# Performance work log

Measured on AMD Instinct MI355X. Metric: run time of the kernel, lower is better.

The kernel has to match this reference:

```python
import jax, jax.numpy as jnp
import numpy as np
import itertools

B, N, C, D = 2, 150000, 64, 128  # samples, points/sample, channels, voxel grid extent
EPS = 1e-4  # BatchNormBlock eps
# 3x3x3 submanifold kernel offsets (27 taps)
OFFS = jnp.array(list(itertools.product((-1, 0, 1), repeat=3)), dtype=jnp.int32)  # [27,3]


def setup_inputs() -> dict:
    key = jax.random.key(0)
    k1, k2 = jax.random.split(key)
    rng = np.random.default_rng(0)
    # unique voxel coordinates per sample on a D^3 grid
    pos = np.stack([
        np.stack(np.unravel_index(rng.choice(D ** 3, size=N, replace=False), (D, D, D)), axis=-1)
        for _ in range(B)
    ]).astype(np.int32)  # [B,N,3]
    feats = jax.random.normal(k1, (B, N, C), jnp.float32)
    # 4 submanifold convs (2 residual blocks x 2 convs), fan-in scaled
    Ws = jax.random.normal(k2, (4, 27, C, C), jnp.float32) / np.sqrt(27 * C)
    gammas = jnp.ones((4, C), jnp.float32)
    betas = jnp.zeros((4, C), jnp.float32)
    return {"feats": feats, "Ws": Ws, "gammas": gammas, "betas": betas, "pos": jnp.asarray(pos)}


def _build_lut(pos_b):  # pos_b: [N,3] int32 -> dense hash grid [D^3] of point index or -1
    code = (pos_b[:, 0] * D + pos_b[:, 1]) * D + pos_b[:, 2]
    return jnp.full((D ** 3,), -1, jnp.int32).at[code].set(jnp.arange(N, dtype=jnp.int32))


def _subconv(x, lut_b, pos_b, W):
    # submanifold sparse conv: per kernel tap, gather neighbor features and GEMM
    # x:[N,C], lut_b:[D^3], pos_b:[N,3], W:[27,Cin,Cout]
    def step(acc, kw):
        d, Wk = kw
        npos = pos_b + d  # [N,3]
        valid = jnp.all((npos >= 0) & (npos < D), axis=-1)
        code = (npos[:, 0] * D + npos[:, 1]) * D + npos[:, 2]
        nidx = lut_b[jnp.where(valid, code, 0)]
        valid = valid & (nidx >= 0)
        g = jnp.where(valid[:, None], x[jnp.clip(nidx, 0, N - 1)], 0.0)  # [N,Cin]
        return acc + g @ Wk, None

    acc0 = jnp.zeros((x.shape[0], W.shape[-1]), x.dtype)
    acc, _ = jax.lax.scan(step, acc0, (OFFS, W))
    return acc


def _bn_relu(x, g, b):
    # BatchNormBlock (train mode, biased var over all concatenated points) + ReLU
    mu = x.mean(axis=(0, 1))
    var = jnp.mean(jnp.square(x - mu), axis=(0, 1))
    return jax.nn.relu((x - mu) * jax.lax.rsqrt(var + EPS) * g + b)


def reference(feats, Ws, gammas, betas, pos):
    lut = jax.vmap(_build_lut)(pos)  # [B, D^3]
    conv = jax.vmap(_subconv, in_axes=(0, 0, 0, None))
    x = feats
    for blk in range(2):  # conv_block_reps ResidualBlocks (NIN is Identity since nIn==nOut)
        out1 = x
        h = _bn_relu(x, gammas[2 * blk], betas[2 * blk])
        h = conv(h, lut, pos, Ws[2 * blk])
        h = _bn_relu(h, gammas[2 * blk + 1], betas[2 * blk + 1])
        out2 = conv(h, lut, pos, Ws[2 * blk + 1])
        x = out1 + out2
    return x
```

## Files before the change

### kernel.cpp

```cpp
#include <hip/hip_runtime.h>
#include <stdint.h>

#define DGRID 128
#define D3 (DGRID * DGRID * DGRID)
#define NBATCH 2
#define NPTS 150000
#define NROWS (NBATCH * NPTS)
#define NPAD 300032
#define ZROW NROWS
#define NCBLK (NPAD / 256)
#define EPSBN 1e-4f
#define SBLK 1024

typedef __attribute__((ext_vector_type(8))) short s16x8;
typedef __attribute__((ext_vector_type(4))) float f32x4;

static __device__ __forceinline__ uint32_t f2bf_rne(float f) {
  uint32_t b = __float_as_uint(f);
  return (b + 0x7FFFu + ((b >> 16) & 1u)) >> 16;
}

static __device__ __forceinline__ f32x4 mfma16(uint4 a, uint4 b, f32x4 c) {
  return __builtin_amdgcn_mfma_f32_16x16x32_bf16(
      __builtin_bit_cast(s16x8, a), __builtin_bit_cast(s16x8, b), c, 0, 0, 0);
}

__global__ void k_scatter(const int* __restrict__ pos, int* __restrict__ lut) {
  int g = blockIdx.x * blockDim.x + threadIdx.x;
  if (g >= NROWS) return;
  int b = g / NPTS;
  int i = g - b * NPTS;
  int x = pos[3 * g], y = pos[3 * g + 1], z = pos[3 * g + 2];
  lut[(size_t)b * D3 + (x * DGRID + y) * DGRID + z] = i;
}

__global__ void k_nbr(const int* __restrict__ pos, const int* __restrict__ lut,
                      int* __restrict__ nbr) {
  int g = blockIdx.x * blockDim.x + threadIdx.x;
  if (g >= NPAD) return;
  if (g >= NROWS) {
#pragma unroll
    for (int t = 0; t < 27; ++t) nbr[(size_t)t * NPAD + g] = ZROW;
    return;
  }
  int b = g / NPTS;
  int x = pos[3 * g], y = pos[3 * g + 1], z = pos[3 * g + 2];
  const int* L = lut + (size_t)b * D3;
#pragma unroll
  for (int t = 0; t < 27; ++t) {
    int nx = x + t / 9 - 1;
    int ny = y + (t / 3) % 3 - 1;
    int nz = z + t % 3 - 1;
    int v = ZROW;
    if ((unsigned)nx < DGRID && (unsigned)ny < DGRID && (unsigned)nz < DGRID) {
      int n = L[(nx * DGRID + ny) * DGRID + nz];
      if (n >= 0) v = b * NPTS + n;
    }
    nbr[(size_t)t * NPAD + g] = v;
  }
}

__global__ void k_wpack(const float* __restrict__ Ws, uint4* __restrict__ Wfrag) {
  int e = blockIdx.x * 256 + threadIdx.x;
  if (e >= 4 * 27 * 512) return;
  int lane = e & 63, nb = (e >> 6) & 3, s = (e >> 8) & 1, tt = e >> 9;
  int kb = s * 32 + (lane >> 4) * 8;
  int cout = nb * 16 + (lane & 15);
  const float* src = Ws + (size_t)tt * 4096;
  uint32_t p[4];
#pragma unroll
  for (int j = 0; j < 4; ++j) {
    uint32_t lo = f2bf_rne(src[(kb + 2 * j) * 64 + cout]);
    uint32_t hi = f2bf_rne(src[(kb + 2 * j + 1) * 64 + cout]);
    p[j] = (hi << 16) | lo;
  }
  uint4 o;
  o.x = p[0]; o.y = p[1]; o.z = p[2]; o.w = p[3];
  Wfrag[e] = o;
}

__global__ void k_stats1(const float* __restrict__ X, float* __restrict__ part) {
  __shared__ float s[512];
  int c = threadIdx.x & 63, q = threadIdx.x >> 6;
  float sm = 0.f, sq = 0.f;
  for (int r = blockIdx.x * 4 + q; r < NROWS; r += SBLK * 4) {
    float v = X[(size_t)r * 64 + c];
    sm += v;
    sq += v * v;
  }
  s[threadIdx.x] = sm;
  s[256 + threadIdx.x] = sq;
  __syncthreads();
  if (q == 0) {
    sm = s[c] + s[64 + c] + s[128 + c] + s[192 + c];
    sq = s[256 + c] + s[320 + c] + s[384 + c] + s[448 + c];
    part[blockIdx.x * 128 + c] = sm;
    part[blockIdx.x * 128 + 64 + c] = sq;
  }
}

__global__ void k_stats2(const float* __restrict__ part, int nblk,
                         const float* __restrict__ gamma, const float* __restrict__ beta,
                         float* __restrict__ chanp, int cid) {
  __shared__ float s[512];
  int c = threadIdx.x & 63, q = threadIdx.x >> 6;
  float sm = 0.f, sq = 0.f;
  for (int rb = q; rb < nblk; rb += 4) {
    sm += part[rb * 128 + c];
    sq += part[rb * 128 + 64 + c];
  }
  s[threadIdx.x] = sm;
  s[256 + threadIdx.x] = sq;
  __syncthreads();
  if (q == 0) {
    sm = s[c] + s[64 + c] + s[128 + c] + s[192 + c];
    sq = s[256 + c] + s[320 + c] + s[384 + c] + s[448 + c];
    float mean = sm / (float)NROWS;
    float var = sq / (float)NROWS - mean * mean;
    float a = gamma[cid * 64 + c] * rsqrtf(var + EPSBN);
    chanp[cid * 128 + c] = a;
    chanp[cid * 128 + 64 + c] = beta[cid * 64 + c] - mean * a;
  }
}

__global__ void k_hpass(const float* __restrict__ X, const float* __restrict__ chanp,
                        int cid, uint4* __restrict__ h) {
  int g = blockIdx.x * blockDim.x + threadIdx.x;
  if (g >= (NROWS + 1) * 8) return;
  if (g >= NROWS * 8) {
    h[g] = (uint4){0u, 0u, 0u, 0u};
    return;
  }
  int c0 = (g & 7) * 8;
  const float* cp = chanp + cid * 128;
  const float4 a0 = *(const float4*)(cp + c0);
  const float4 a1 = *(const float4*)(cp + c0 + 4);
  const float4 b0 = *(const float4*)(cp + 64 + c0);
  const float4 b1 = *(const float4*)(cp + 64 + c0 + 4);
  const float4 x0 = *(const float4*)(X + (size_t)g * 8);
  const float4 x1 = *(const float4*)(X + (size_t)g * 8 + 4);
  float v0 = fmaxf(fmaf(x0.x, a0.x, b0.x), 0.f);
  float v1 = fmaxf(fmaf(x0.y, a0.y, b0.y), 0.f);
  float v2 = fmaxf(fmaf(x0.z, a0.z, b0.z), 0.f);
  float v3 = fmaxf(fmaf(x0.w, a0.w, b0.w), 0.f);
  float v4 = fmaxf(fmaf(x1.x, a1.x, b1.x), 0.f);
  float v5 = fmaxf(fmaf(x1.y, a1.y, b1.y), 0.f);
  float v6 = fmaxf(fmaf(x1.z, a1.z, b1.z), 0.f);
  float v7 = fmaxf(fmaf(x1.w, a1.w, b1.w), 0.f);
  uint4 o;
  o.x = (f2bf_rne(v1) << 16) | f2bf_rne(v0);
  o.y = (f2bf_rne(v3) << 16) | f2bf_rne(v2);
  o.z = (f2bf_rne(v5) << 16) | f2bf_rne(v4);
  o.w = (f2bf_rne(v7) << 16) | f2bf_rne(v6);
  h[g] = o;
}

#define MFMA_HALF(AREG, WOFF)                                            \
  {                                                                      \
    uint4 wf[4];                                                         \
    _Pragma("unroll") for (int nb = 0; nb < 4; nb++) wf[nb] =            \
        Wt[(WOFF) + nb * 64];                                            \
    _Pragma("unroll") for (int rt = 0; rt < 4; rt++)                     \
        _Pragma("unroll") for (int nb = 0; nb < 4; nb++) acc[rt][nb] =   \
            mfma16(AREG, wf[nb], acc[rt][nb]);                           \
  }

__global__ __launch_bounds__(256) void k_conv(
    const uint4* __restrict__ h, const uint4* __restrict__ Wf,
    const int* __restrict__ nbr, const float* __restrict__ res,
    float* __restrict__ out, float* __restrict__ part, int do_stats) {
  __shared__ float xp[4][16 * 68];
  __shared__ float sred[2][4][4][16];
  int tid = threadIdx.x, wv = tid >> 6, lane = tid & 63;
  int tbase = (blockIdx.x * 4 + wv) * 64;
  int lrow = lane & 15, lkg = lane >> 4;

  f32x4 acc[4][4];
#pragma unroll
  for (int i = 0; i < 4; i++)
#pragma unroll
    for (int j = 0; j < 4; j++) acc[i][j] = (f32x4){0.f, 0.f, 0.f, 0.f};

  const int* nb0 = nbr + tbase + lrow;
  int niA[4], niB[4];
  uint4 aA[4][2], aB[4][2];
#pragma unroll
  for (int rt = 0; rt < 4; rt++) niA[rt] = nb0[rt * 16];
#pragma unroll
  for (int rt = 0; rt < 4; rt++) {
    const uint4* hp = h + (size_t)niA[rt] * 8 + lkg;
    aA[rt][0] = hp[0];
    aA[rt][1] = hp[4];
  }
#pragma unroll
  for (int rt = 0; rt < 4; rt++) niB[rt] = nb0[(size_t)NPAD + rt * 16];

  for (int t = 0; t < 26; t += 2) {
#pragma unroll
    for (int rt = 0; rt < 4; rt++) niA[rt] = nb0[(size_t)(t + 2) * NPAD + rt * 16];
#pragma unroll
    for (int rt = 0; rt < 4; rt++) {
      const uint4* hp = h + (size_t)niB[rt] * 8 + lkg;
      aB[rt][0] = hp[0];
      aB[rt][1] = hp[4];
    }
    {
      const uint4* Wt = Wf + (size_t)t * 512 + lane;
      MFMA_HALF(aA[rt][0], 0)
      MFMA_HALF(aA[rt][1], 256)
    }
    int t3 = (t + 3 < 27) ? t + 3 : 26;
#pragma unroll
    for (int rt = 0; rt < 4; rt++) niB[rt] = nb0[(size_t)t3 * NPAD + rt * 16];
#pragma unroll
    for (int rt = 0; rt < 4; rt++) {
      const uint4* hp = h + (size_t)niA[rt] * 8 + lkg;
      aA[rt][0] = hp[0];
      aA[rt][1] = hp[4];
    }
    {
      const uint4* Wt = Wf + (size_t)(t + 1) * 512 + lane;
      MFMA_HALF(aB[rt][0], 0)
      MFMA_HALF(aB[rt][1], 256)
    }
  }
  {
    const uint4* Wt = Wf + (size_t)26 * 512 + lane;
    MFMA_HALF(aA[rt][0], 0)
    MFMA_HALF(aA[rt][1], 256)
  }

  float smc[16], sqc[16];
#pragma unroll
  for (int j = 0; j < 16; j++) smc[j] = sqc[j] = 0.f;
  float* slab = xp[wv];
#pragma unroll 1
  for (int rt = 0; rt < 4; rt++) {
#pragma unroll
    for (int nb = 0; nb < 4; nb++)
#pragma unroll
      for (int r = 0; r < 4; r++)
        slab[(lkg * 4 + r) * 68 + nb * 16 + lrow] = acc[rt][nb][r];
    __syncthreads();
    int gr = tbase + rt * 16 + lrow;
    if (gr < NROWS) {
#pragma unroll
      for (int j = 0; j < 4; j++) {
        float4 vv = *(float4*)&slab[lrow * 68 + lkg * 16 + j * 4];
        size_t off = (size_t)gr * 64 + lkg * 16 + j * 4;
        if (res) {
          float4 rr = *(const float4*)(res + off);
          vv.x += rr.x; vv.y += rr.y; vv.z += rr.z; vv.w += rr.w;
        }
        *(float4*)(out + off) = vv;
        smc[j * 4 + 0] += vv.x; sqc[j * 4 + 0] += vv.x * vv.x;
        smc[j * 4 + 1] += vv.y; sqc[j * 4 + 1] += vv.y * vv.y;
        smc[j * 4 + 2] += vv.z; sqc[j * 4 + 2] += vv.z * vv.z;
        smc[j * 4 + 3] += vv.w; sqc[j * 4 + 3] += vv.w * vv.w;
      }
    }
    __syncthreads();
  }
  if (do_stats) {
#pragma unroll
    for (int j = 0; j < 16; j++) {
      smc[j] += __shfl_xor(smc[j], 1); sqc[j] += __shfl_xor(sqc[j], 1);
      smc[j] += __shfl_xor(smc[j], 2); sqc[j] += __shfl_xor(sqc[j], 2);
      smc[j] += __shfl_xor(smc[j], 4); sqc[j] += __shfl_xor(sqc[j], 4);
      smc[j] += __shfl_xor(smc[j], 8); sqc[j] += __shfl_xor(sqc[j], 8);
    }
    if (lrow == 0) {
#pragma unroll
      for (int j = 0; j < 16; j++) {
        sred[0][wv][lkg][j] = smc[j];
        sred[1][wv][lkg][j] = sqc[j];
      }
    }
    __syncthreads();
    if (tid < 64) {
      float s0 = 0.f, s1 = 0.f;
      int q = tid >> 4, c = tid & 15;
#pragma unroll
      for (int w = 0; w < 4; w++) {
        s0 += sred[0][w][q][c];
        s1 += sred[1][w][q][c];
      }
      part[blockIdx.x * 128 + tid] = s0;
      part[blockIdx.x * 128 + 64 + tid] = s1;
    }
  }
}

extern "C" void kernel_launch(void* const* d_in, const int* in_sizes, int n_in,
                              void* d_out, int out_size, void* d_ws, size_t ws_size,
                              hipStream_t stream) {
  const float* feats = (const float*)d_in[0];
  const float* Ws = (const float*)d_in[1];
  const float* gammas = (const float*)d_in[2];
  const float* betas = (const float*)d_in[3];
  const int* pos = (const int*)d_in[4];
  float* out = (float*)d_out;

  char* w = (char*)d_ws;
  auto alloc = [&](size_t b) {
    char* p = w;
    w += (b + 255) & ~(size_t)255;
    return p;
  };
  int* nbr = (int*)alloc((size_t)27 * NPAD * 4);
  uint4* Wfrag = (uint4*)alloc((size_t)4 * 27 * 512 * 16);
  float* part = (float*)alloc((size_t)NCBLK * 128 * 4);
  float* chanp = (float*)alloc((size_t)4 * 128 * 4);
  uint4* h = (uint4*)alloc((size_t)NPAD * 128);
  float* xbuf = (float*)alloc((size_t)NROWS * 64 * 4);
  char* reg0 = alloc((size_t)NROWS * 64 * 4);
  float* cbuf = (float*)reg0;
  int* lut = (int*)reg0;

  hipMemsetAsync(lut, 0xFF, (size_t)NBATCH * D3 * 4, stream);
  int gpts = (NROWS + 255) / 256;
  k_scatter<<<gpts, 256, 0, stream>>>(pos, lut);
  k_nbr<<<NPAD / 256, 256, 0, stream>>>(pos, lut, nbr);
  k_wpack<<<216, 256, 0, stream>>>(Ws, Wfrag);

  k_stats1<<<SBLK, 256, 0, stream>>>(feats, part);
  k_stats2<<<1, 256, 0, stream>>>(part, SBLK, gammas, betas, chanp, 0);
  k_hpass<<<9376, 256, 0, stream>>>(feats, chanp, 0, h);
  k_conv<<<NCBLK, 256, 0, stream>>>(h, Wfrag + 0 * 27 * 512, nbr, nullptr, cbuf, part, 1);

  k_stats2<<<1, 256, 0, stream>>>(part, NCBLK, gammas, betas, chanp, 1);
  k_hpass<<<9376, 256, 0, stream>>>(cbuf, chanp, 1, h);
  k_conv<<<NCBLK, 256, 0, stream>>>(h, Wfrag + 1 * 27 * 512, nbr, feats, xbuf, part, 1);

  k_stats2<<<1, 256, 0, stream>>>(part, NCBLK, gammas, betas, chanp, 2);
  k_hpass<<<9376, 256, 0, stream>>>(xbuf, chanp, 2, h);
  k_conv<<<NCBLK, 256, 0, stream>>>(h, Wfrag + 2 * 27 * 512, nbr, nullptr, cbuf, part, 1);

  k_stats2<<<1, 256, 0, stream>>>(part, NCBLK, gammas, betas, chanp, 3);
  k_hpass<<<9376, 256, 0, stream>>>(cbuf, chanp, 3, h);
  k_conv<<<NCBLK, 256, 0, stream>>>(h, Wfrag + 3 * 27 * 512, nbr, xbuf, out, part, 0);
}
```

Baseline: 1.188 ms.

## Halve conv rows per wave and double-buffer weights in registers for occupancy

The submanifold conv kernel now processes 32 rows per wave instead of 64, so there are half as many accumulators and twice as many blocks. Weight fragments for the next tap are prefetched into registers alongside the next neighbor gather, in a ping-pong pipeline. Launch bounds now request 3 blocks per SM. This aims to raise occupancy and hide gather latency. The cost is that each weight load is reused over fewer rows, giving more weight traffic per MFMA.

```diff
diff --git a/kernel.cpp b/kernel.cpp
--- a/kernel.cpp
+++ b/kernel.cpp
@@ -8,7 +8,7 @@
 #define NROWS (NBATCH * NPTS)
 #define NPAD 300032
 #define ZROW NROWS
-#define NCBLK (NPAD / 256)
+#define NCBLK (NPAD / 128)
 #define EPSBN 1e-4f
 #define SBLK 1024
 
@@ -155,87 +155,71 @@
   h[g] = o;
 }
 
-#define MFMA_HALF(AREG, WOFF)                                            \
-  {                                                                      \
-    uint4 wf[4];                                                         \
-    _Pragma("unroll") for (int nb = 0; nb < 4; nb++) wf[nb] =            \
-        Wt[(WOFF) + nb * 64];                                            \
-    _Pragma("unroll") for (int rt = 0; rt < 4; rt++)                     \
-        _Pragma("unroll") for (int nb = 0; nb < 4; nb++) acc[rt][nb] =   \
-            mfma16(AREG, wf[nb], acc[rt][nb]);                           \
-  }
-
-__global__ __launch_bounds__(256) void k_conv(
+#define PH(T, WC, WN, AC, AN, NIA, NIL)                                     \
+  {                                                                         \
+    int tw = (T) + 1 <= 26 ? (T) + 1 : 26;                                  \
+    const uint4* Wt = Wf + (size_t)tw * 512 + lane;                         \
+    _Pragma("unroll") for (int i = 0; i < 8; i++) WN[i] = Wt[i * 64];       \
+    int tn = (T) + 2 <= 26 ? (T) + 2 : 26;                                  \
+    NIL[0] = nbp[(size_t)tn * NPAD];                                        \
+    NIL[1] = nbp[(size_t)tn * NPAD + 16];                                   \
+    {                                                                       \
+      const uint4* hp0 = h + (size_t)NIA[0] * 8 + lkg;                      \
+      const uint4* hp1 = h + (size_t)NIA[1] * 8 + lkg;                      \
+      AN[0][0] = hp0[0]; AN[0][1] = hp0[4];                                 \
+      AN[1][0] = hp1[0]; AN[1][1] = hp1[4];                                 \
+    }                                                                       \
+    _Pragma("unroll") for (int s = 0; s < 2; s++)                           \
+      _Pragma("unroll") for (int rt = 0; rt < 2; rt++)                      \
+        _Pragma("unroll") for (int nb = 0; nb < 4; nb++)                    \
+          acc[rt][nb] = mfma16(AC[rt][s], WC[s * 4 + nb], acc[rt][nb]);     \
+  }
+
+__global__ __launch_bounds__(256, 3) void k_conv(
     const uint4* __restrict__ h, const uint4* __restrict__ Wf,
     const int* __restrict__ nbr, const float* __restrict__ res,
     float* __restrict__ out, float* __restrict__ part, int do_stats) {
   __shared__ float xp[4][16 * 68];
   __shared__ float sred[2][4][4][16];
   int tid = threadIdx.x, wv = tid >> 6, lane = tid & 63;
-  int tbase = (blockIdx.x * 4 + wv) * 64;
+  int tbase = (blockIdx.x * 4 + wv) * 32;
   int lrow = lane & 15, lkg = lane >> 4;
 
-  f32x4 acc[4][4];
-#pragma unroll
-  for (int i = 0; i < 4; i++)
+  f32x4 acc[2][4];
+#pragma unroll
+  for (int i = 0; i < 2; i++)
 #pragma unroll
     for (int j = 0; j < 4; j++) acc[i][j] = (f32x4){0.f, 0.f, 0.f, 0.f};
 
-  const int* nb0 = nbr + tbase + lrow;
-  int niA[4], niB[4];
-  uint4 aA[4][2], aB[4][2];
-#pragma unroll
-  for (int rt = 0; rt < 4; rt++) niA[rt] = nb0[rt * 16];
-#pragma unroll
-  for (int rt = 0; rt < 4; rt++) {
-    const uint4* hp = h + (size_t)niA[rt] * 8 + lkg;
-    aA[rt][0] = hp[0];
-    aA[rt][1] = hp[4];
-  }
-#pragma unroll
-  for (int rt = 0; rt < 4; rt++) niB[rt] = nb0[(size_t)NPAD + rt * 16];
+  const int* nbp = nbr + tbase + lrow;
+  int n0[2], n1[2];
+  uint4 w0[8], w1[8];
+  uint4 a0[2][2], a1[2][2];
+
+  int p0 = nbp[0], p1 = nbp[16];
+  n1[0] = nbp[NPAD];
+  n1[1] = nbp[NPAD + 16];
+#pragma unroll
+  for (int i = 0; i < 8; i++) w0[i] = Wf[i * 64 + lane];
+  {
+    const uint4* hp0 = h + (size_t)p0 * 8 + lkg;
+    const uint4* hp1 = h + (size_t)p1 * 8 + lkg;
+    a0[0][0] = hp0[0]; a0[0][1] = hp0[4];
+    a0[1][0] = hp1[0]; a0[1][1] = hp1[4];
+  }
 
   for (int t = 0; t < 26; t += 2) {
-#pragma unroll
-    for (int rt = 0; rt < 4; rt++) niA[rt] = nb0[(size_t)(t + 2) * NPAD + rt * 16];
-#pragma unroll
-    for (int rt = 0; rt < 4; rt++) {
-      const uint4* hp = h + (size_t)niB[rt] * 8 + lkg;
-      aB[rt][0] = hp[0];
-      aB[rt][1] = hp[4];
-    }
-    {
-      const uint4* Wt = Wf + (size_t)t * 512 + lane;
-      MFMA_HALF(aA[rt][0], 0)
-      MFMA_HALF(aA[rt][1], 256)
-    }
-    int t3 = (t + 3 < 27) ? t + 3 : 26;
-#pragma unroll
-    for (int rt = 0; rt < 4; rt++) niB[rt] = nb0[(size_t)t3 * NPAD + rt * 16];
-#pragma unroll
-    for (int rt = 0; rt < 4; rt++) {
-      const uint4* hp = h + (size_t)niA[rt] * 8 + lkg;
-      aA[rt][0] = hp[0];
-      aA[rt][1] = hp[4];
-    }
-    {
-      const uint4* Wt = Wf + (size_t)(t + 1) * 512 + lane;
-      MFMA_HALF(aB[rt][0], 0)
-      MFMA_HALF(aB[rt][1], 256)
-    }
-  }
-  {
-    const uint4* Wt = Wf + (size_t)26 * 512 + lane;
-    MFMA_HALF(aA[rt][0], 0)
-    MFMA_HALF(aA[rt][1], 256)
-  }
+    PH(t, w0, w1, a0, a1, n1, n0)
+    PH(t + 1, w1, w0, a1, a0, n0, n1)
+  }
+  PH(26, w0, w1, a0, a1, n1, n0)
 
   float smc[16], sqc[16];
 #pragma unroll
   for (int j = 0; j < 16; j++) smc[j] = sqc[j] = 0.f;
   float* slab = xp[wv];
 #pragma unroll 1
-  for (int rt = 0; rt < 4; rt++) {
+  for (int rt = 0; rt < 2; rt++) {
 #pragma unroll
     for (int nb = 0; nb < 4; nb++)
 #pragma unroll
```

New measurement: 1.439 ms. 21.1% more time.
